# Kernel optimization log

Measured on AMD Instinct MI355X. Metric: run time of the kernel, lower is better.

The kernel has to match this reference:

```python
import jax, jax.numpy as jnp
import numpy as np
from math import sqrt

D_MODEL = 1024
N_HEADS = 16
D_V = D_MODEL // N_HEADS
D_FF = 4 * D_MODEL
EPS = 1e-5


def setup_inputs() -> dict:
    key = jax.random.key(0)
    ks = jax.random.split(key, 12)
    N, L = 2, 2048
    s = 0.02
    return {
        'queries': jax.random.normal(ks[0], (N, L, D_MODEL), jnp.float32),
        'keys': jax.random.normal(ks[1], (N, L, D_MODEL), jnp.float32),
        'values': jax.random.normal(ks[2], (N, L, D_MODEL), jnp.float32),
        'mask': jnp.ones((N, 1, 1, L), jnp.int32),
        'fc_w': jax.random.normal(ks[3], (D_MODEL, D_MODEL), jnp.float32) * s,
        'fc_b': jnp.zeros((D_MODEL,), jnp.float32),
        'ln1_g': jnp.ones((D_MODEL,), jnp.float32),
        'ln1_b': jnp.zeros((D_MODEL,), jnp.float32),
        'ff_w1': jax.random.normal(ks[4], (D_MODEL, D_FF), jnp.float32) * s,
        'ff_b1': jnp.zeros((D_FF,), jnp.float32),
        'ff_w2': jax.random.normal(ks[5], (D_FF, D_MODEL), jnp.float32) * s,
        'ff_b2': jnp.zeros((D_MODEL,), jnp.float32),
        'ln2_g': jnp.ones((D_MODEL,), jnp.float32),
        'ln2_b': jnp.zeros((D_MODEL,), jnp.float32),
    }


def layer_norm(x, g, b):
    mu = jnp.mean(x, axis=-1, keepdims=True)
    var = jnp.mean(jnp.square(x - mu), axis=-1, keepdims=True)
    return (x - mu) * jax.lax.rsqrt(var + EPS) * g + b


def reference(queries, keys, values, mask, fc_w, fc_b, ln1_g, ln1_b,
              ff_w1, ff_b1, ff_w2, ff_b2, ln2_g, ln2_b):
    N, Lq, _ = queries.shape
    Lk = keys.shape[1]
    # NOTE: the original module never applies its Q/K/V linear layers; raw
    # inputs are reshaped directly into heads.
    q = queries.reshape(N, Lq, N_HEADS, D_V).transpose(0, 2, 1, 3)  # nhqd
    k = keys.reshape(N, Lk, N_HEADS, D_V)                           # nlhd
    v = values.reshape(N, Lk, N_HEADS, D_V)                         # nlhd
    energy = jnp.einsum('nhqd,nlhd->nhql', q, k)
    energy = jnp.where(mask == 0, -jnp.inf, energy)
    # original scales by sqrt(d_model), not sqrt(d_v)
    attn = jax.nn.softmax(energy / sqrt(D_MODEL), axis=-1)
    out = jnp.einsum('nhql,nlhd->nqhd', attn, v).reshape(N, Lq, D_MODEL)
    attention = out @ fc_w + fc_b
    x1 = layer_norm(attention + queries, ln1_g, ln1_b)
    fc = jax.nn.relu(x1 @ ff_w1 + ff_b1) @ ff_w2 + ff_b2
    x2 = layer_norm(fc + x1, ln2_g, ln2_b)
    return x2
```

## Files before the change

### kernel.cpp

```cpp
#include <hip/hip_runtime.h>
#include <stdint.h>

typedef unsigned short u16;
typedef __bf16 bf16x8 __attribute__((ext_vector_type(8), may_alias));
typedef float f32x4 __attribute__((ext_vector_type(4), may_alias));

typedef void __attribute__((address_space(1))) as1_void;
typedef void __attribute__((address_space(3))) as3_void;

#define MFMA16 __builtin_amdgcn_mfma_f32_16x16x32_bf16

#define SBAR()                                \
    do {                                      \
        asm volatile("" ::: "memory");        \
        __builtin_amdgcn_s_barrier();         \
        asm volatile("" ::: "memory");        \
    } while (0)
#define WAITV(n) asm volatile("s_waitcnt vmcnt(" #n ")" ::: "memory")
#define WAITL0() asm volatile("s_waitcnt lgkmcnt(0)" ::: "memory")

__device__ __forceinline__ void async_copy16(const void* g, void* l) {
    __builtin_amdgcn_global_load_lds((as1_void*)g, (as3_void*)l, 16, 0, 0);
}

__device__ __forceinline__ u16 f2bf(float f) {
    union { float f; unsigned u; } c; c.f = f;
    unsigned u = c.u;
    u += 0x7fffu + ((u >> 16) & 1u);
    return (u16)(u >> 16);
}

__global__ __launch_bounds__(256) void cast_f32_bf16(
    const float* __restrict__ in, u16* __restrict__ out, int n4, float scale) {
    int i = blockIdx.x * 256 + threadIdx.x;
    if (i < n4) {
        f32x4 v = *(const f32x4*)&in[(size_t)i * 4];
        ushort4 o;
        o.x = f2bf(v[0] * scale); o.y = f2bf(v[1] * scale);
        o.z = f2bf(v[2] * scale); o.w = f2bf(v[3] * scale);
        *(ushort4*)&out[(size_t)i * 4] = o;
    }
}

__global__ __launch_bounds__(256) void transpose_cast(
    const float* __restrict__ in, u16* __restrict__ out, int R, int C) {
    __shared__ float tile[64][65];
    const float* inb = in + (size_t)blockIdx.z * R * C;
    u16* outb = out + (size_t)blockIdx.z * R * C;
    int t = threadIdx.x;
    int c0 = blockIdx.x * 64, r0 = blockIdx.y * 64;
    int tr = t >> 4, tc = (t & 15) * 4;
#pragma unroll
    for (int p = 0; p < 4; ++p) {
        int r = tr + p * 16;
        f32x4 v = *(const f32x4*)&inb[(size_t)(r0 + r) * C + c0 + tc];
        tile[r][tc] = v[0]; tile[r][tc + 1] = v[1];
        tile[r][tc + 2] = v[2]; tile[r][tc + 3] = v[3];
    }
    __syncthreads();
    int wc = t >> 4, wr = (t & 15) * 4;
#pragma unroll
    for (int p = 0; p < 4; ++p) {
        int cl = wc + p * 16;
        ushort4 o;
        o.x = f2bf(tile[wr + 0][cl]); o.y = f2bf(tile[wr + 1][cl]);
        o.z = f2bf(tile[wr + 2][cl]); o.w = f2bf(tile[wr + 3][cl]);
        *(ushort4*)&outb[(size_t)(c0 + cl) * R + r0 + wr] = o;
    }
}

__global__ __launch_bounds__(256) void flash_attn(
    const u16* __restrict__ Q, const u16* __restrict__ Kb,
    const u16* __restrict__ VT, const int* __restrict__ mask,
    u16* __restrict__ O) {
    __shared__ u16 kls[2][8192];
    __shared__ u16 vls[8192];
    __shared__ u16 pls[8][2048];

    const int bid = blockIdx.x;
    const int qt = bid & 15;
    const int h = (bid >> 4) & 15;
    const int n = bid >> 8;
    const int t = threadIdx.x;
    const int w = t >> 6, lane = t & 63;
    const int m16 = lane & 15, quad = lane >> 4;

    const size_t qrowA = (size_t)(n * 2048 + qt * 128 + w * 16 + m16);
    const size_t qrowB = qrowA + 64;
    bf16x8 qfA0 = *(const bf16x8*)&Q[qrowA * 1024 + h * 64 + quad * 8];
    bf16x8 qfA1 = *(const bf16x8*)&Q[qrowA * 1024 + h * 64 + 32 + quad * 8];
    bf16x8 qfB0 = *(const bf16x8*)&Q[qrowB * 1024 + h * 64 + quad * 8];
    bf16x8 qfB1 = *(const bf16x8*)&Q[qrowB * 1024 + h * 64 + 32 + quad * 8];

    const int* maskn = mask + n * 2048;
    int allones;
    {
        int ok = 1;
#pragma unroll
        for (int i = 0; i < 8; ++i) {
            int4 mv = *(const int4*)&maskn[lane * 32 + i * 4];
            ok &= (mv.x != 0) & (mv.y != 0) & (mv.z != 0) & (mv.w != 0);
        }
        allones = __all(ok);
    }

    f32x4 otA[4] = {}, otB[4] = {};
    f32x4 sumA = {}, sumB = {};

    const u16* Kbase = Kb + (size_t)(n * 2048) * 1024 + h * 64;
    const u16* Vbase = VT + (size_t)(n * 1024 + h * 64) * 2048;
    u16* pwA = &pls[w * 2][0];
    u16* pwB = &pls[w * 2 + 1][0];

#pragma unroll
    for (int i = 0; i < 4; ++i) {
        int e = w * 4 + i;
        async_copy16(&Kbase[(size_t)((e >> 1) * 16 + m16) * 1024 + (e & 1) * 32 + quad * 8],
                     &kls[0][e * 512]);
    }
    __syncthreads();

    for (int kt = 0; kt < 16; ++kt) {
        const u16* kcur = kls[kt & 1];
        if (kt + 1 < 16) {
            u16* knext = kls[(kt + 1) & 1];
#pragma unroll
            for (int i = 0; i < 4; ++i) {
                int e = w * 4 + i;
                async_copy16(&Kbase[(size_t)((kt + 1) * 128 + (e >> 1) * 16 + m16) * 1024 +
                                    (e & 1) * 32 + quad * 8], &knext[e * 512]);
            }
        }
#pragma unroll
        for (int i = 0; i < 4; ++i) {
            int e = w * 4 + i;
            async_copy16(&Vbase[(size_t)((e >> 2) * 16 + m16) * 2048 + kt * 128 +
                                (e & 3) * 32 + quad * 8], &vls[e * 512]);
        }

        f32x4 sA[8] = {}, sB[8] = {};
#pragma unroll
        for (int ct = 0; ct < 8; ++ct) {
            bf16x8 a0 = *(const bf16x8*)&kcur[(ct * 2 + 0) * 512 + lane * 8];
            bf16x8 a1 = *(const bf16x8*)&kcur[(ct * 2 + 1) * 512 + lane * 8];
            sA[ct] = MFMA16(a0, qfA0, sA[ct], 0, 0, 0);
            sA[ct] = MFMA16(a1, qfA1, sA[ct], 0, 0, 0);
            sB[ct] = MFMA16(a0, qfB0, sB[ct], 0, 0, 0);
            sB[ct] = MFMA16(a1, qfB1, sB[ct], 0, 0, 0);
        }

        if (allones) {
#pragma unroll
            for (int ct = 0; ct < 8; ++ct) {
                int c = ct * 2 + (quad >> 1);
                int off = m16 * 128 + (((c ^ m16) & 15) << 3) + (quad & 1) * 4;
                {
                    float p0 = __builtin_amdgcn_exp2f(sA[ct][0]);
                    float p1 = __builtin_amdgcn_exp2f(sA[ct][1]);
                    float p2 = __builtin_amdgcn_exp2f(sA[ct][2]);
                    float p3 = __builtin_amdgcn_exp2f(sA[ct][3]);
                    sumA[0] += p0; sumA[1] += p1; sumA[2] += p2; sumA[3] += p3;
                    unsigned lo = __builtin_amdgcn_perm(__float_as_uint(p1), __float_as_uint(p0), 0x07060302);
                    unsigned hi = __builtin_amdgcn_perm(__float_as_uint(p3), __float_as_uint(p2), 0x07060302);
                    *(uint2*)&pwA[off] = make_uint2(lo, hi);
                }
                {
                    float p0 = __builtin_amdgcn_exp2f(sB[ct][0]);
                    float p1 = __builtin_amdgcn_exp2f(sB[ct][1]);
                    float p2 = __builtin_amdgcn_exp2f(sB[ct][2]);
                    float p3 = __builtin_amdgcn_exp2f(sB[ct][3]);
                    sumB[0] += p0; sumB[1] += p1; sumB[2] += p2; sumB[3] += p3;
                    unsigned lo = __builtin_amdgcn_perm(__float_as_uint(p1), __float_as_uint(p0), 0x07060302);
                    unsigned hi = __builtin_amdgcn_perm(__float_as_uint(p3), __float_as_uint(p2), 0x07060302);
                    *(uint2*)&pwB[off] = make_uint2(lo, hi);
                }
            }
        } else {
#pragma unroll
            for (int ct = 0; ct < 8; ++ct) {
                const int4 mv = *(const int4*)&maskn[kt * 128 + ct * 16 + quad * 4];
                int c = ct * 2 + (quad >> 1);
                int off = m16 * 128 + (((c ^ m16) & 15) << 3) + (quad & 1) * 4;
                {
                    float p0 = __builtin_amdgcn_exp2f(sA[ct][0]) * (mv.x ? 1.f : 0.f);
                    float p1 = __builtin_amdgcn_exp2f(sA[ct][1]) * (mv.y ? 1.f : 0.f);
                    float p2 = __builtin_amdgcn_exp2f(sA[ct][2]) * (mv.z ? 1.f : 0.f);
                    float p3 = __builtin_amdgcn_exp2f(sA[ct][3]) * (mv.w ? 1.f : 0.f);
                    sumA[0] += p0; sumA[1] += p1; sumA[2] += p2; sumA[3] += p3;
                    unsigned lo = __builtin_amdgcn_perm(__float_as_uint(p1), __float_as_uint(p0), 0x07060302);
                    unsigned hi = __builtin_amdgcn_perm(__float_as_uint(p3), __float_as_uint(p2), 0x07060302);
                    *(uint2*)&pwA[off] = make_uint2(lo, hi);
                }
                {
                    float p0 = __builtin_amdgcn_exp2f(sB[ct][0]) * (mv.x ? 1.f : 0.f);
                    float p1 = __builtin_amdgcn_exp2f(sB[ct][1]) * (mv.y ? 1.f : 0.f);
                    float p2 = __builtin_amdgcn_exp2f(sB[ct][2]) * (mv.z ? 1.f : 0.f);
                    float p3 = __builtin_amdgcn_exp2f(sB[ct][3]) * (mv.w ? 1.f : 0.f);
                    sumB[0] += p0; sumB[1] += p1; sumB[2] += p2; sumB[3] += p3;
                    unsigned lo = __builtin_amdgcn_perm(__float_as_uint(p1), __float_as_uint(p0), 0x07060302);
                    unsigned hi = __builtin_amdgcn_perm(__float_as_uint(p3), __float_as_uint(p2), 0x07060302);
                    *(uint2*)&pwB[off] = make_uint2(lo, hi);
                }
            }
        }

        __syncthreads();

        bf16x8 pfA[4], pfB[4];
#pragma unroll
        for (int kc2 = 0; kc2 < 4; ++kc2) {
            int off = m16 * 128 + ((((kc2 * 4 + quad) ^ m16) & 15) << 3);
            pfA[kc2] = *(const bf16x8*)&pwA[off];
            pfB[kc2] = *(const bf16x8*)&pwB[off];
        }
#pragma unroll
        for (int kc2 = 0; kc2 < 4; ++kc2) {
#pragma unroll
            for (int dt = 0; dt < 4; ++dt) {
                bf16x8 vf = *(const bf16x8*)&vls[(dt * 4 + kc2) * 512 + lane * 8];
                otA[dt] = MFMA16(vf, pfA[kc2], otA[dt], 0, 0, 0);
                otB[dt] = MFMA16(vf, pfB[kc2], otB[dt], 0, 0, 0);
            }
        }
        __syncthreads();
    }

    float lA = (sumA[0] + sumA[1]) + (sumA[2] + sumA[3]);
    float lB = (sumB[0] + sumB[1]) + (sumB[2] + sumB[3]);
    lA += __shfl_xor(lA, 16); lA += __shfl_xor(lA, 32);
    lB += __shfl_xor(lB, 16); lB += __shfl_xor(lB, 32);
    float invA = 1.f / fmaxf(lA, 1e-30f);
    float invB = 1.f / fmaxf(lB, 1e-30f);

    const size_t obA = qrowA * 1024 + h * 64;
    const size_t obB = qrowB * 1024 + h * 64;
#pragma unroll
    for (int dt = 0; dt < 4; ++dt) {
        unsigned lo = (unsigned)f2bf(otA[dt][0] * invA) | ((unsigned)f2bf(otA[dt][1] * invA) << 16);
        unsigned hi = (unsigned)f2bf(otA[dt][2] * invA) | ((unsigned)f2bf(otA[dt][3] * invA) << 16);
        *(uint2*)&O[obA + dt * 16 + quad * 4] = make_uint2(lo, hi);
        lo = (unsigned)f2bf(otB[dt][0] * invB) | ((unsigned)f2bf(otB[dt][1] * invB) << 16);
        hi = (unsigned)f2bf(otB[dt][2] * invB) | ((unsigned)f2bf(otB[dt][3] * invB) << 16);
        *(uint2*)&O[obB + dt * 16 + quad * 4] = make_uint2(lo, hi);
    }
}

template <int BM, int BN, int RELU, int OUTBF, int SPLITK>
__global__ __launch_bounds__(256) void gemm_bt(
    const u16* __restrict__ A, const u16* __restrict__ Bt,
    const float* __restrict__ bias, void* __restrict__ Cout,
    void* __restrict__ Cout1, int M, int N, int K) {
    constexpr int MI = BM / 32;
    constexpr int NJ = BN / 32;
    __shared__ u16 sm[2][(BM + BN) * 64];
    const int lane = threadIdx.x & 63;
    const int w = threadIdx.x >> 6;
    const int m16 = lane & 15, quad = lane >> 4;
    const int nBn = N / BN;
    int bid = blockIdx.x;
    int slice = 0;
    if (SPLITK > 1) {
        const int nblk = (M / BM) * nBn;
        slice = bid / nblk;
        bid = bid - slice * nblk;
    }
    const int bm = bid / nBn, bn = bid % nBn;
    const int r2 = w >> 1, c2 = w & 1;
    const int Ks = K / SPLITK;
    const int kOff = slice * Ks;

    const u16* Abase = A + (size_t)(bm * BM + m16) * K + quad * 8;
    const u16* Bbase = Bt + (size_t)(bn * BN + m16) * K + quad * 8;

    auto stage = [&](int buf, int k0) {
        u16* smA = &sm[buf][0];
        u16* smB = smA + BM * 64;
#pragma unroll
        for (int i = 0; i < MI; ++i) {
            int e = w * MI + i;
            async_copy16(&Abase[(size_t)((e >> 1) * 16) * K + k0 + (e & 1) * 32], &smA[e * 512]);
        }
#pragma unroll
        for (int i = 0; i < NJ; ++i) {
            int e = w * NJ + i;
            async_copy16(&Bbase[(size_t)((e >> 1) * 16) * K + k0 + (e & 1) * 32], &smB[e * 512]);
        }
    };

    f32x4 acc[MI][NJ] = {};
    const int nK = Ks >> 6;
    stage(0, kOff);
    __syncthreads();
    for (int kt = 0; kt < nK; ++kt) {
        if (kt + 1 < nK) stage((kt + 1) & 1, kOff + ((kt + 1) << 6));
        const u16* smA = &sm[kt & 1][0];
        const u16* smB = smA + BM * 64;
#pragma unroll
        for (int kc = 0; kc < 2; ++kc) {
            bf16x8 a[MI], b[NJ];
#pragma unroll
            for (int i = 0; i < MI; ++i)
                a[i] = *(const bf16x8*)&smA[((r2 * MI + i) * 2 + kc) * 512 + lane * 8];
#pragma unroll
            for (int j = 0; j < NJ; ++j)
                b[j] = *(const bf16x8*)&smB[((c2 * NJ + j) * 2 + kc) * 512 + lane * 8];
#pragma unroll
            for (int i = 0; i < MI; ++i)
#pragma unroll
                for (int j = 0; j < NJ; ++j)
                    acc[i][j] = MFMA16(a[i], b[j], acc[i][j], 0, 0, 0);
        }
        __syncthreads();
    }
    float bv[NJ];
#pragma unroll
    for (int j = 0; j < NJ; ++j)
        bv[j] = (SPLITK == 1 || slice == 0)
                    ? bias[bn * BN + c2 * (BN / 2) + j * 16 + m16] : 0.f;
    void* Csel = (SPLITK > 1 && slice != 0) ? Cout1 : Cout;
#pragma unroll
    for (int i = 0; i < MI; ++i) {
        int row0 = bm * BM + r2 * (BM / 2) + i * 16 + quad * 4;
#pragma unroll
        for (int j = 0; j < NJ; ++j) {
            int col = bn * BN + c2 * (BN / 2) + j * 16 + m16;
#pragma unroll
            for (int r = 0; r < 4; ++r) {
                float v = acc[i][j][r] + bv[j];
                if (RELU) v = fmaxf(v, 0.f);
                size_t idx = (size_t)(row0 + r) * N + col;
                if (OUTBF) ((u16*)Cout)[idx] = f2bf(v);
                else ((float*)Csel)[idx] = v;
                (void)Csel;
            }
        }
    }
}

template <int RELU, int OUTBF, int SPLITK>
__global__ __launch_bounds__(512, 2) void gemm_8ph(
    const u16* __restrict__ A, const u16* __restrict__ Bt,
    const float* __restrict__ bias,
    void* __restrict__ C0, void* __restrict__ C1,
    void* __restrict__ C2a, void* __restrict__ C2b, void* __restrict__ C3,
    int M, int N, int K) {
    __shared__ u16 sm[2][2][16384];
    const int t = threadIdx.x;
    const int w = t >> 6, lane = t & 63;
    const int m16 = lane & 15, quad = lane >> 4;
    const int wm = w >> 2, wn = w & 3;
    const int nBn = N >> 8;
    int bid = blockIdx.x, slice = 0;
    if (SPLITK > 1) {
        const int nblk = (M >> 8) * nBn;
        slice = bid / nblk;
        bid -= slice * nblk;
    }
    const int bm = bid / nBn, bn = bid % nBn;
    const int Ks = K / SPLITK;
    const int nK = Ks >> 6, nIter = nK >> 1;
    const u16* Abase = A + (size_t)(bm * 256 + m16) * K + slice * Ks + quad * 8;
    const u16* Bbase = Bt + (size_t)(bn * 256 + m16) * K + slice * Ks + quad * 8;

    auto stage_ht = [&](int h) {
        if (h < 4 * nK) {
            const int kt = h >> 2, q = h & 3;
            const u16* base = (q < 2) ? Abase : Bbase;
            u16* lds = &sm[kt & 1][q >> 1][0];
            const int h0 = (q & 1) * 16;
#pragma unroll
            for (int i = 0; i < 2; ++i) {
                const int e = h0 + i * 8 + w;
                async_copy16(&base[(size_t)((e >> 1) * 16) * K + (size_t)kt * 64 + (e & 1) * 32],
                             &lds[e * 512]);
            }
        }
    };
    auto ldsA = [&](int buf, int mf, int kc) {
        return *(const bf16x8*)&sm[buf][0][((wm * 8 + mf) * 2 + kc) * 512 + lane * 8];
    };
    auto ldsB = [&](int buf, int nf, int kc) {
        return *(const bf16x8*)&sm[buf][1][((wn * 4 + nf) * 2 + kc) * 512 + lane * 8];
    };

    f32x4 acc[8][4] = {};
    bf16x8 a0[4][2], a1[4][2], b[4][2];

#define QUAD(Ar, BO, MO, NO)                                                    \
    do {                                                                        \
        __builtin_amdgcn_s_setprio(1);                                          \
        _Pragma("unroll") for (int mi = 0; mi < 4; ++mi)                        \
            _Pragma("unroll") for (int nj = 0; nj < 2; ++nj)                    \
                _Pragma("unroll") for (int kc = 0; kc < 2; ++kc)                \
                    acc[(MO) + mi][(NO) + nj] =                                 \
                        MFMA16(Ar[mi][kc], b[(BO) + nj][kc],                    \
                               acc[(MO) + mi][(NO) + nj], 0, 0, 0);             \
        __builtin_amdgcn_s_setprio(0);                                          \
    } while (0)

    stage_ht(0); stage_ht(1); stage_ht(2); stage_ht(3);
    WAITV(4);
    stage_ht(4); stage_ht(5); stage_ht(6);
    WAITV(6);
    SBAR();

    for (int it = 0; it < nIter; ++it) {
        const int hb = it * 8;
#pragma unroll
        for (int mf = 0; mf < 4; ++mf) { a0[mf][0] = ldsA(0, mf, 0); a0[mf][1] = ldsA(0, mf, 1); }
#pragma unroll
        for (int nf = 0; nf < 2; ++nf) { b[nf][0] = ldsB(0, nf, 0); b[nf][1] = ldsB(0, nf, 1); }
        stage_ht(hb + 7);
        SBAR(); WAITL0();
        QUAD(a0, 0, 0, 0);
        SBAR();
#pragma unroll
        for (int mf = 0; mf < 4; ++mf) { a1[mf][0] = ldsA(0, mf + 4, 0); a1[mf][1] = ldsA(0, mf + 4, 1); }
#pragma unroll
        for (int nf = 0; nf < 2; ++nf) { b[2 + nf][0] = ldsB(0, 2 + nf, 0); b[2 + nf][1] = ldsB(0, 2 + nf, 1); }
        stage_ht(hb + 8);
        SBAR(); WAITL0();
        QUAD(a0, 2, 0, 2);
        SBAR();
        stage_ht(hb + 9);
        SBAR(); WAITL0();
        QUAD(a1, 2, 4, 2);
        SBAR();
        stage_ht(hb + 10);
        if (it == nIter - 1) { WAITV(0); } else { WAITV(6); }
        SBAR(); WAITL0();
        QUAD(a1, 0, 4, 0);
        SBAR();
#pragma unroll
        for (int mf = 0; mf < 4; ++mf) { a0[mf][0] = ldsA(1, mf, 0); a0[mf][1] = ldsA(1, mf, 1); }
#pragma unroll
        for (int nf = 0; nf < 2; ++nf) { b[nf][0] = ldsB(1, nf, 0); b[nf][1] = ldsB(1, nf, 1); }
        stage_ht(hb + 11);
        SBAR(); WAITL0();
        QUAD(a0, 0, 0, 0);
        SBAR();
#pragma unroll
        for (int mf = 0; mf < 4; ++mf) { a1[mf][0] = ldsA(1, mf + 4, 0); a1[mf][1] = ldsA(1, mf + 4, 1); }
#pragma unroll
        for (int nf = 0; nf < 2; ++nf) { b[2 + nf][0] = ldsB(1, 2 + nf, 0); b[2 + nf][1] = ldsB(1, 2 + nf, 1); }
        stage_ht(hb + 12);
        SBAR(); WAITL0();
        QUAD(a0, 2, 0, 2);
        SBAR();
        stage_ht(hb + 13);
        SBAR(); WAITL0();
        QUAD(a1, 2, 4, 2);
        SBAR();
        stage_ht(hb + 14);
        if (it + 1 < nIter) { WAITV(6); } else { WAITV(0); }
        SBAR(); WAITL0();
        QUAD(a1, 0, 4, 0);
        SBAR();
    }
#undef QUAD

    float bv[4];
#pragma unroll
    for (int nf = 0; nf < 4; ++nf)
        bv[nf] = (SPLITK == 1 || slice == 0) ? bias[bn * 256 + wn * 64 + nf * 16 + m16] : 0.f;
    void* Csel = C0;
    int rowAdj = 0;
    if (SPLITK > 1) {
        if (slice == 1) Csel = C1;
        else if (slice == 3) Csel = C3;
        else if (slice == 2) {
            const int half = M >> 9;
            if (bm < half) Csel = C2a;
            else { Csel = C2b; rowAdj = M >> 1; }
        }
    }
    const int colb = bn * 256 + wn * 64 + m16;
#pragma unroll
    for (int mf = 0; mf < 8; ++mf) {
        const int row0 = bm * 256 + wm * 128 + mf * 16 + quad * 4 - rowAdj;
#pragma unroll
        for (int nf = 0; nf < 4; ++nf) {
#pragma unroll
            for (int r = 0; r < 4; ++r) {
                float v = acc[mf][nf][r] + bv[nf];
                if (RELU) v = fmaxf(v, 0.f);
                size_t idx = (size_t)(row0 + r) * N + colb + nf * 16;
                if (OUTBF) ((u16*)Csel)[idx] = f2bf(v);
                else ((float*)Csel)[idx] = v;
            }
        }
    }
}

__global__ __launch_bounds__(256) void ln_residual(
    const float* x, const float* x2,
    const float* x3a, const float* x3b, const float* x4,
    const float* __restrict__ res,
    const float* __restrict__ g, const float* __restrict__ b,
    float* out_f32, u16* __restrict__ out_bf16) {
    __shared__ float smr[8];
    int row = blockIdx.x;
    int t = threadIdx.x;
    f32x4 xv = *(const f32x4*)&x[(size_t)row * 1024 + t * 4];
    f32x4 rv = *(const f32x4*)&res[(size_t)row * 1024 + t * 4];
    xv += rv;
    if (x2) xv += *(const f32x4*)&x2[(size_t)row * 1024 + t * 4];
    if (x3a) {
        const float* p = (row < 2048) ? x3a + (size_t)row * 1024
                                      : x3b + (size_t)(row - 2048) * 1024;
        xv += *(const f32x4*)&p[t * 4];
    }
    if (x4) xv += *(const f32x4*)&x4[(size_t)row * 1024 + t * 4];
    float s = xv[0] + xv[1] + xv[2] + xv[3];
    float ss = xv[0] * xv[0] + xv[1] * xv[1] + xv[2] * xv[2] + xv[3] * xv[3];
#pragma unroll
    for (int d = 1; d < 64; d <<= 1) {
        s += __shfl_xor(s, d);
        ss += __shfl_xor(ss, d);
    }
    int w = t >> 6, lane = t & 63;
    if (lane == 0) { smr[w] = s; smr[4 + w] = ss; }
    __syncthreads();
    s = smr[0] + smr[1] + smr[2] + smr[3];
    ss = smr[4] + smr[5] + smr[6] + smr[7];
    float mu = s * (1.f / 1024.f);
    float var = ss * (1.f / 1024.f) - mu * mu;
    float rs = rsqrtf(var + 1e-5f);
    f32x4 gv = *(const f32x4*)&g[t * 4];
    f32x4 bv = *(const f32x4*)&b[t * 4];
    f32x4 y;
#pragma unroll
    for (int i = 0; i < 4; ++i) y[i] = (xv[i] - mu) * rs * gv[i] + bv[i];
    *(f32x4*)&out_f32[(size_t)row * 1024 + t * 4] = y;
    if (out_bf16) {
        ushort4 o;
        o.x = f2bf(y[0]); o.y = f2bf(y[1]); o.z = f2bf(y[2]); o.w = f2bf(y[3]);
        *(ushort4*)&out_bf16[(size_t)row * 1024 + t * 4] = o;
    }
}

extern "C" void kernel_launch(void* const* d_in, const int* in_sizes, int n_in,
                              void* d_out, int out_size, void* d_ws, size_t ws_size,
                              hipStream_t stream) {
    const float* q = (const float*)d_in[0];
    const float* k = (const float*)d_in[1];
    const float* v = (const float*)d_in[2];
    const int* mask = (const int*)d_in[3];
    const float* fc_b = (const float*)d_in[5];
    const float* ln1_g = (const float*)d_in[6];
    const float* ln1_b = (const float*)d_in[7];
    const float* ff_b1 = (const float*)d_in[9];
    const float* ff_b2 = (const float*)d_in[11];
    const float* ln2_g = (const float*)d_in[12];
    const float* ln2_b = (const float*)d_in[13];
    const float* fc_w = (const float*)d_in[4];
    const float* ff_w1 = (const float*)d_in[8];
    const float* ff_w2 = (const float*)d_in[10];

    char* ws = (char*)d_ws;
    const size_t MB = 1024 * 1024;
    u16* qbf = (u16*)(ws + 0);
    u16* kbf = (u16*)(ws + 8 * MB);
    u16* vT  = (u16*)(ws + 16 * MB);
    u16* ao  = (u16*)(ws + 24 * MB);
    u16* hbuf = (u16*)(ws + 0);
    u16* fcwT = (u16*)(ws + 32 * MB);
    u16* w1T  = (u16*)(ws + 34 * MB);
    u16* w2T  = (u16*)(ws + 42 * MB);
    float* attn_raw = (float*)(ws + 50 * MB);
    float* fc_raw   = (float*)(ws + 50 * MB);
    float* x1   = (float*)(ws + 66 * MB);
    u16* x1bf   = (u16*)(ws + 82 * MB);
    float* attn_rawB = (float*)(ws + 0);
    float* fcB  = (float*)(ws + 90 * MB);
    float* fcC_lo = (float*)(ws + 32 * MB);
    float* fcC_hi = (float*)(ws + 82 * MB);
    const bool big = ws_size >= 106 * MB;

    const float k2 = 0.03125f * 1.44269504088896340736f;

    cast_f32_bf16<<<4096, 256, 0, stream>>>(q, qbf, 1048576, k2);
    cast_f32_bf16<<<4096, 256, 0, stream>>>(k, kbf, 1048576, 1.0f);
    transpose_cast<<<dim3(16, 32, 2), 256, 0, stream>>>(v, vT, 2048, 1024);
    transpose_cast<<<dim3(16, 16, 1), 256, 0, stream>>>(fc_w, fcwT, 1024, 1024);
    transpose_cast<<<dim3(64, 16, 1), 256, 0, stream>>>(ff_w1, w1T, 1024, 4096);
    transpose_cast<<<dim3(16, 64, 1), 256, 0, stream>>>(ff_w2, w2T, 4096, 1024);

    flash_attn<<<512, 256, 0, stream>>>(qbf, kbf, vT, mask, ao);

    gemm_bt<128, 128, 0, 0, 2><<<32 * 8 * 2, 256, 0, stream>>>(
        ao, fcwT, fc_b, attn_raw, attn_rawB, 4096, 1024, 1024);
    ln_residual<<<4096, 256, 0, stream>>>(attn_raw, attn_rawB, nullptr, nullptr, nullptr,
                                          q, ln1_g, ln1_b, x1, x1bf);

    gemm_8ph<1, 1, 1><<<256, 512, 0, stream>>>(
        x1bf, w1T, ff_b1, hbuf, nullptr, nullptr, nullptr, nullptr, 4096, 4096, 1024);

    if (big) {
        gemm_8ph<0, 0, 4><<<256, 512, 0, stream>>>(
            hbuf, w2T, ff_b2, fc_raw, fcB, fcC_lo, fcC_hi, (float*)d_out,
            4096, 1024, 4096);
        ln_residual<<<4096, 256, 0, stream>>>(fc_raw, fcB, fcC_lo, fcC_hi, (float*)d_out,
                                              x1, ln2_g, ln2_b, (float*)d_out, (u16*)nullptr);
    } else {
        gemm_bt<64, 128, 0, 0, 1><<<64 * 8, 256, 0, stream>>>(
            hbuf, w2T, ff_b2, fc_raw, nullptr, 4096, 1024, 4096);
        ln_residual<<<4096, 256, 0, stream>>>(fc_raw, nullptr, nullptr, nullptr, nullptr,
                                              x1, ln2_g, ln2_b, (float*)d_out, (u16*)nullptr);
    }
}
```

Measured before the change: 381.1 us.

## Add 128x256 split-K GEMM, shorten prefetch pipeline, swizzle block order

```diff
diff --git a/kernel.cpp b/kernel.cpp
--- a/kernel.cpp
+++ b/kernel.cpp
@@ -329,20 +329,17 @@
                 float v = acc[i][j][r] + bv[j];
                 if (RELU) v = fmaxf(v, 0.f);
                 size_t idx = (size_t)(row0 + r) * N + col;
-                if (OUTBF) ((u16*)Cout)[idx] = f2bf(v);
+                if (OUTBF) ((u16*)Csel)[idx] = f2bf(v);
                 else ((float*)Csel)[idx] = v;
-                (void)Csel;
-            }
-        }
-    }
-}
-
-template <int RELU, int OUTBF, int SPLITK>
+            }
+        }
+    }
+}
+
+template <int RELU, int OUTBF>
 __global__ __launch_bounds__(512, 2) void gemm_8ph(
     const u16* __restrict__ A, const u16* __restrict__ Bt,
-    const float* __restrict__ bias,
-    void* __restrict__ C0, void* __restrict__ C1,
-    void* __restrict__ C2a, void* __restrict__ C2b, void* __restrict__ C3,
+    const float* __restrict__ bias, void* __restrict__ Cout,
     int M, int N, int K) {
     __shared__ u16 sm[2][2][16384];
     const int t = threadIdx.x;
@@ -350,24 +347,19 @@
     const int m16 = lane & 15, quad = lane >> 4;
     const int wm = w >> 2, wn = w & 3;
     const int nBn = N >> 8;
-    int bid = blockIdx.x, slice = 0;
-    if (SPLITK > 1) {
-        const int nblk = (M >> 8) * nBn;
-        slice = bid / nblk;
-        bid -= slice * nblk;
-    }
-    const int bm = bid / nBn, bn = bid % nBn;
-    const int Ks = K / SPLITK;
-    const int nK = Ks >> 6, nIter = nK >> 1;
-    const u16* Abase = A + (size_t)(bm * 256 + m16) * K + slice * Ks + quad * 8;
-    const u16* Bbase = Bt + (size_t)(bn * 256 + m16) * K + slice * Ks + quad * 8;
-
-    auto stage_ht = [&](int h) {
-        if (h < 4 * nK) {
-            const int kt = h >> 2, q = h & 3;
-            const u16* base = (q < 2) ? Abase : Bbase;
-            u16* lds = &sm[kt & 1][q >> 1][0];
-            const int h0 = (q & 1) * 16;
+    const int nblk = (M >> 8) * nBn;
+    const int o = blockIdx.x;
+    const int v = (o & 7) * (nblk >> 3) + (o >> 3);
+    const int bm = v / nBn, bn = v - bm * nBn;
+    const int nK = K >> 6, nIter = nK >> 1;
+    const u16* Abase = A + (size_t)(bm * 256 + m16) * K + quad * 8;
+    const u16* Bbase = Bt + (size_t)(bn * 256 + m16) * K + quad * 8;
+
+    auto stage_ht = [&](int kt, int part) {
+        if (kt < nK) {
+            const u16* base = (part < 2) ? Abase : Bbase;
+            u16* lds = &sm[kt & 1][part >> 1][0];
+            const int h0 = (part & 1) * 16;
 #pragma unroll
             for (int i = 0; i < 2; ++i) {
                 const int e = h0 + i * 8 + w;
@@ -386,118 +378,240 @@
     f32x4 acc[8][4] = {};
     bf16x8 a0[4][2], a1[4][2], b[4][2];
 
-#define QUAD(Ar, BO, MO, NO)                                                    \
+#define QUAD8(Ar, BO, MO)                                                       \
     do {                                                                        \
         __builtin_amdgcn_s_setprio(1);                                          \
         _Pragma("unroll") for (int mi = 0; mi < 4; ++mi)                        \
             _Pragma("unroll") for (int nj = 0; nj < 2; ++nj)                    \
                 _Pragma("unroll") for (int kc = 0; kc < 2; ++kc)                \
-                    acc[(MO) + mi][(NO) + nj] =                                 \
+                    acc[(MO) + mi][(BO) + nj] =                                 \
                         MFMA16(Ar[mi][kc], b[(BO) + nj][kc],                    \
-                               acc[(MO) + mi][(NO) + nj], 0, 0, 0);             \
+                               acc[(MO) + mi][(BO) + nj], 0, 0, 0);             \
         __builtin_amdgcn_s_setprio(0);                                          \
     } while (0)
 
-    stage_ht(0); stage_ht(1); stage_ht(2); stage_ht(3);
+    stage_ht(0, 0); stage_ht(0, 1); stage_ht(0, 2); stage_ht(0, 3);
+    stage_ht(1, 0); stage_ht(1, 1);
     WAITV(4);
-    stage_ht(4); stage_ht(5); stage_ht(6);
-    WAITV(6);
     SBAR();
 
     for (int it = 0; it < nIter; ++it) {
-        const int hb = it * 8;
+        const int T1 = 2 * it + 1, T2 = 2 * it + 2, T3 = 2 * it + 3;
+        const bool last = (it + 1 == nIter);
 #pragma unroll
         for (int mf = 0; mf < 4; ++mf) { a0[mf][0] = ldsA(0, mf, 0); a0[mf][1] = ldsA(0, mf, 1); }
 #pragma unroll
         for (int nf = 0; nf < 2; ++nf) { b[nf][0] = ldsB(0, nf, 0); b[nf][1] = ldsB(0, nf, 1); }
-        stage_ht(hb + 7);
-        SBAR(); WAITL0();
-        QUAD(a0, 0, 0, 0);
+        stage_ht(T1, 2);
+        SBAR(); WAITL0();
+        QUAD8(a0, 0, 0);
         SBAR();
 #pragma unroll
         for (int mf = 0; mf < 4; ++mf) { a1[mf][0] = ldsA(0, mf + 4, 0); a1[mf][1] = ldsA(0, mf + 4, 1); }
 #pragma unroll
         for (int nf = 0; nf < 2; ++nf) { b[2 + nf][0] = ldsB(0, 2 + nf, 0); b[2 + nf][1] = ldsB(0, 2 + nf, 1); }
-        stage_ht(hb + 8);
-        SBAR(); WAITL0();
-        QUAD(a0, 2, 0, 2);
-        SBAR();
-        stage_ht(hb + 9);
-        SBAR(); WAITL0();
-        QUAD(a1, 2, 4, 2);
-        SBAR();
-        stage_ht(hb + 10);
-        if (it == nIter - 1) { WAITV(0); } else { WAITV(6); }
-        SBAR(); WAITL0();
-        QUAD(a1, 0, 4, 0);
+        stage_ht(T1, 3);
+        SBAR(); WAITL0();
+        QUAD8(a0, 2, 0);
+        SBAR();
+        stage_ht(T2, 0);
+        SBAR(); WAITL0();
+        QUAD8(a1, 2, 4);
+        SBAR();
+        stage_ht(T2, 1);
+        if (last) { WAITV(0); } else { WAITV(4); }
+        SBAR(); WAITL0();
+        QUAD8(a1, 0, 4);
         SBAR();
 #pragma unroll
         for (int mf = 0; mf < 4; ++mf) { a0[mf][0] = ldsA(1, mf, 0); a0[mf][1] = ldsA(1, mf, 1); }
 #pragma unroll
         for (int nf = 0; nf < 2; ++nf) { b[nf][0] = ldsB(1, nf, 0); b[nf][1] = ldsB(1, nf, 1); }
-        stage_ht(hb + 11);
-        SBAR(); WAITL0();
-        QUAD(a0, 0, 0, 0);
+        stage_ht(T2, 2);
+        SBAR(); WAITL0();
+        QUAD8(a0, 0, 0);
         SBAR();
 #pragma unroll
         for (int mf = 0; mf < 4; ++mf) { a1[mf][0] = ldsA(1, mf + 4, 0); a1[mf][1] = ldsA(1, mf + 4, 1); }
 #pragma unroll
         for (int nf = 0; nf < 2; ++nf) { b[2 + nf][0] = ldsB(1, 2 + nf, 0); b[2 + nf][1] = ldsB(1, 2 + nf, 1); }
-        stage_ht(hb + 12);
-        SBAR(); WAITL0();
-        QUAD(a0, 2, 0, 2);
-        SBAR();
-        stage_ht(hb + 13);
-        SBAR(); WAITL0();
-        QUAD(a1, 2, 4, 2);
-        SBAR();
-        stage_ht(hb + 14);
-        if (it + 1 < nIter) { WAITV(6); } else { WAITV(0); }
-        SBAR(); WAITL0();
-        QUAD(a1, 0, 4, 0);
-        SBAR();
-    }
-#undef QUAD
+        stage_ht(T2, 3);
+        SBAR(); WAITL0();
+        QUAD8(a0, 2, 0);
+        SBAR();
+        stage_ht(T3, 0);
+        SBAR(); WAITL0();
+        QUAD8(a1, 2, 4);
+        SBAR();
+        stage_ht(T3, 1);
+        if (last) { WAITV(0); } else { WAITV(4); }
+        SBAR(); WAITL0();
+        QUAD8(a1, 0, 4);
+        SBAR();
+    }
+#undef QUAD8
 
     float bv[4];
 #pragma unroll
     for (int nf = 0; nf < 4; ++nf)
-        bv[nf] = (SPLITK == 1 || slice == 0) ? bias[bn * 256 + wn * 64 + nf * 16 + m16] : 0.f;
-    void* Csel = C0;
-    int rowAdj = 0;
-    if (SPLITK > 1) {
-        if (slice == 1) Csel = C1;
-        else if (slice == 3) Csel = C3;
-        else if (slice == 2) {
-            const int half = M >> 9;
-            if (bm < half) Csel = C2a;
-            else { Csel = C2b; rowAdj = M >> 1; }
-        }
-    }
+        bv[nf] = bias[bn * 256 + wn * 64 + nf * 16 + m16];
     const int colb = bn * 256 + wn * 64 + m16;
 #pragma unroll
     for (int mf = 0; mf < 8; ++mf) {
-        const int row0 = bm * 256 + wm * 128 + mf * 16 + quad * 4 - rowAdj;
+        const int row0 = bm * 256 + wm * 128 + mf * 16 + quad * 4;
 #pragma unroll
         for (int nf = 0; nf < 4; ++nf) {
 #pragma unroll
             for (int r = 0; r < 4; ++r) {
-                float v = acc[mf][nf][r] + bv[nf];
-                if (RELU) v = fmaxf(v, 0.f);
+                float vv = acc[mf][nf][r] + bv[nf];
+                if (RELU) vv = fmaxf(vv, 0.f);
                 size_t idx = (size_t)(row0 + r) * N + colb + nf * 16;
-                if (OUTBF) ((u16*)Csel)[idx] = f2bf(v);
-                else ((float*)Csel)[idx] = v;
+                if (OUTBF) ((u16*)Cout)[idx] = f2bf(vv);
+                else ((float*)Cout)[idx] = vv;
+            }
+        }
+    }
+}
+
+template <int RELU, int OUTBF, int SPLITK>
+__global__ __launch_bounds__(512, 2) void gemm_sk(
+    const u16* __restrict__ A, const u16* __restrict__ Bt,
+    const float* __restrict__ bias,
+    void* __restrict__ C0, void* __restrict__ C1,
+    int M, int N, int K) {
+    __shared__ u16 smA[2][8192];
+    __shared__ u16 smB[2][16384];
+    const int t = threadIdx.x;
+    const int w = t >> 6, lane = t & 63;
+    const int m16 = lane & 15, quad = lane >> 4;
+    const int wm = w >> 2, wn = w & 3;
+    const int nBn = N >> 8;
+    const int nblk = (M >> 7) * nBn * SPLITK;
+    const int o = blockIdx.x;
+    const int v = (o & 7) * (nblk >> 3) + (o >> 3);
+    const int gsz = nBn * SPLITK;
+    const int bm = v / gsz;
+    const int rr = v - bm * gsz;
+    const int slice = rr / nBn;
+    const int bn = rr - slice * nBn;
+    const int Ks = K / SPLITK;
+    const int nK = Ks >> 6, nIter = nK >> 1;
+    const u16* Abase = A + (size_t)(bm * 128 + m16) * K + slice * Ks + quad * 8;
+    const u16* Bbase = Bt + (size_t)(bn * 256 + m16) * K + slice * Ks + quad * 8;
+
+    auto stage_u = [&](int kt, int part) {
+        if (kt < nK) {
+#pragma unroll
+            for (int i = 0; i < 2; ++i) {
+                const int idx = i * 8 + w;
+                int e;
+                const u16* base;
+                u16* lds;
+                if (part == 0) {
+                    e = idx; base = Abase; lds = &smA[kt & 1][0];
+                } else {
+                    const int rbs = idx >> 1;
+                    const int rb = ((rbs >> 1) << 2) | (rbs & 1) | ((part == 2) ? 2 : 0);
+                    e = rb * 2 + (idx & 1);
+                    base = Bbase; lds = &smB[kt & 1][0];
+                }
+                async_copy16(&base[(size_t)((e >> 1) * 16) * K + (size_t)kt * 64 + (e & 1) * 32],
+                             &lds[e * 512]);
+            }
+        }
+    };
+    auto ldsA = [&](int buf, int mf, int kc) {
+        return *(const bf16x8*)&smA[buf][((wm * 4 + mf) * 2 + kc) * 512 + lane * 8];
+    };
+    auto ldsB = [&](int buf, int nf, int kc) {
+        return *(const bf16x8*)&smB[buf][((wn * 4 + nf) * 2 + kc) * 512 + lane * 8];
+    };
+
+    f32x4 acc[4][4] = {};
+    bf16x8 af[4][2], bf[2][2];
+
+#define QUADS(NO)                                                               \
+    do {                                                                        \
+        __builtin_amdgcn_s_setprio(1);                                          \
+        _Pragma("unroll") for (int mi = 0; mi < 4; ++mi)                        \
+            _Pragma("unroll") for (int nj = 0; nj < 2; ++nj)                    \
+                _Pragma("unroll") for (int kc = 0; kc < 2; ++kc)                \
+                    acc[mi][(NO) + nj] =                                        \
+                        MFMA16(af[mi][kc], bf[nj][kc],                          \
+                               acc[mi][(NO) + nj], 0, 0, 0);                    \
+        __builtin_amdgcn_s_setprio(0);                                          \
+    } while (0)
+
+    stage_u(0, 0); stage_u(0, 1); stage_u(0, 2);
+    stage_u(1, 0); stage_u(1, 1);
+    WAITV(4);
+    SBAR();
+
+    for (int it = 0; it < nIter; ++it) {
+        const int T1 = 2 * it + 1, T2 = 2 * it + 2, T3 = 2 * it + 3;
+        const bool last = (it + 1 == nIter);
+#pragma unroll
+        for (int mf = 0; mf < 4; ++mf) { af[mf][0] = ldsA(0, mf, 0); af[mf][1] = ldsA(0, mf, 1); }
+#pragma unroll
+        for (int nf = 0; nf < 2; ++nf) { bf[nf][0] = ldsB(0, nf, 0); bf[nf][1] = ldsB(0, nf, 1); }
+        stage_u(T1, 2);
+        SBAR(); WAITL0();
+        QUADS(0);
+        SBAR();
+#pragma unroll
+        for (int nf = 0; nf < 2; ++nf) { bf[nf][0] = ldsB(0, 2 + nf, 0); bf[nf][1] = ldsB(0, 2 + nf, 1); }
+        stage_u(T2, 0); stage_u(T2, 1);
+        if (last) { WAITV(0); } else { WAITV(4); }
+        SBAR(); WAITL0();
+        QUADS(2);
+        SBAR();
+#pragma unroll
+        for (int mf = 0; mf < 4; ++mf) { af[mf][0] = ldsA(1, mf, 0); af[mf][1] = ldsA(1, mf, 1); }
+#pragma unroll
+        for (int nf = 0; nf < 2; ++nf) { bf[nf][0] = ldsB(1, nf, 0); bf[nf][1] = ldsB(1, nf, 1); }
+        stage_u(T2, 2);
+        SBAR(); WAITL0();
+        QUADS(0);
+        SBAR();
+#pragma unroll
+        for (int nf = 0; nf < 2; ++nf) { bf[nf][0] = ldsB(1, 2 + nf, 0); bf[nf][1] = ldsB(1, 2 + nf, 1); }
+        stage_u(T3, 0); stage_u(T3, 1);
+        if (last) { WAITV(0); } else { WAITV(4); }
+        SBAR(); WAITL0();
+        QUADS(2);
+        SBAR();
+    }
+#undef QUADS
+
+    float bv[4];
+#pragma unroll
+    for (int nf = 0; nf < 4; ++nf)
+        bv[nf] = (SPLITK == 1 || slice == 0)
+                     ? bias[bn * 256 + wn * 64 + nf * 16 + m16] : 0.f;
+    void* Csel = (SPLITK > 1 && slice != 0) ? C1 : C0;
+    const int colb = bn * 256 + wn * 64 + m16;
+#pragma unroll
+    for (int mf = 0; mf < 4; ++mf) {
+        const int row0 = bm * 128 + wm * 64 + mf * 16 + quad * 4;
+#pragma unroll
+        for (int nf = 0; nf < 4; ++nf) {
+#pragma unroll
+            for (int r = 0; r < 4; ++r) {
+                float vv = acc[mf][nf][r] + bv[nf];
+                if (RELU) vv = fmaxf(vv, 0.f);
+                size_t idx = (size_t)(row0 + r) * N + colb + nf * 16;
+                if (OUTBF) ((u16*)Csel)[idx] = f2bf(vv);
+                else ((float*)Csel)[idx] = vv;
             }
         }
     }
 }
 
 __global__ __launch_bounds__(256) void ln_residual(
-    const float* x, const float* x2,
-    const float* x3a, const float* x3b, const float* x4,
+    const float* __restrict__ x, const float* x2,
     const float* __restrict__ res,
     const float* __restrict__ g, const float* __restrict__ b,
-    float* out_f32, u16* __restrict__ out_bf16) {
+    float* __restrict__ out_f32, u16* __restrict__ out_bf16) {
     __shared__ float smr[8];
     int row = blockIdx.x;
     int t = threadIdx.x;
@@ -505,12 +619,6 @@
     f32x4 rv = *(const f32x4*)&res[(size_t)row * 1024 + t * 4];
     xv += rv;
     if (x2) xv += *(const f32x4*)&x2[(size_t)row * 1024 + t * 4];
-    if (x3a) {
-        const float* p = (row < 2048) ? x3a + (size_t)row * 1024
-                                      : x3b + (size_t)(row - 2048) * 1024;
-        xv += *(const f32x4*)&p[t * 4];
-    }
-    if (x4) xv += *(const f32x4*)&x4[(size_t)row * 1024 + t * 4];
     float s = xv[0] + xv[1] + xv[2] + xv[3];
     float ss = xv[0] * xv[0] + xv[1] * xv[1] + xv[2] * xv[2] + xv[3] * xv[3];
 #pragma unroll
@@ -573,8 +681,6 @@
     u16* x1bf   = (u16*)(ws + 82 * MB);
     float* attn_rawB = (float*)(ws + 0);
     float* fcB  = (float*)(ws + 90 * MB);
-    float* fcC_lo = (float*)(ws + 32 * MB);
-    float* fcC_hi = (float*)(ws + 82 * MB);
     const bool big = ws_size >= 106 * MB;
 
     const float k2 = 0.03125f * 1.44269504088896340736f;
@@ -588,24 +694,22 @@
 
     flash_attn<<<512, 256, 0, stream>>>(qbf, kbf, vT, mask, ao);
 
-    gemm_bt<128, 128, 0, 0, 2><<<32 * 8 * 2, 256, 0, stream>>>(
+    gemm_sk<0, 0, 2><<<256, 512, 0, stream>>>(
         ao, fcwT, fc_b, attn_raw, attn_rawB, 4096, 1024, 1024);
-    ln_residual<<<4096, 256, 0, stream>>>(attn_raw, attn_rawB, nullptr, nullptr, nullptr,
-                                          q, ln1_g, ln1_b, x1, x1bf);
-
-    gemm_8ph<1, 1, 1><<<256, 512, 0, stream>>>(
-        x1bf, w1T, ff_b1, hbuf, nullptr, nullptr, nullptr, nullptr, 4096, 4096, 1024);
+    ln_residual<<<4096, 256, 0, stream>>>(attn_raw, attn_rawB, q, ln1_g, ln1_b, x1, x1bf);
+
+    gemm_8ph<1, 1><<<256, 512, 0, stream>>>(
+        x1bf, w1T, ff_b1, hbuf, 4096, 4096, 1024);
 
     if (big) {
-        gemm_8ph<0, 0, 4><<<256, 512, 0, stream>>>(
-            hbuf, w2T, ff_b2, fc_raw, fcB, fcC_lo, fcC_hi, (float*)d_out,
-            4096, 1024, 4096);
-        ln_residual<<<4096, 256, 0, stream>>>(fc_raw, fcB, fcC_lo, fcC_hi, (float*)d_out,
-                                              x1, ln2_g, ln2_b, (float*)d_out, (u16*)nullptr);
+        gemm_sk<0, 0, 2><<<256, 512, 0, stream>>>(
+            hbuf, w2T, ff_b2, fc_raw, fcB, 4096, 1024, 4096);
+        ln_residual<<<4096, 256, 0, stream>>>(fc_raw, fcB, x1, ln2_g, ln2_b,
+                                              (float*)d_out, (u16*)nullptr);
     } else {
         gemm_bt<64, 128, 0, 0, 1><<<64 * 8, 256, 0, stream>>>(
             hbuf, w2T, ff_b2, fc_raw, nullptr, 4096, 1024, 4096);
-        ln_residual<<<4096, 256, 0, stream>>>(fc_raw, nullptr, nullptr, nullptr, nullptr,
-                                              x1, ln2_g, ln2_b, (float*)d_out, (u16*)nullptr);
-    }
-}
+        ln_residual<<<4096, 256, 0, stream>>>(fc_raw, nullptr, x1, ln2_g, ln2_b,
+                                              (float*)d_out, (u16*)nullptr);
+    }
+}
```

New measurement: 390.6 us. +2.5%, slower.
